# Kernel optimization log

Measured on AMD Instinct MI355X. Metric: run time of the kernel, lower is better.

Reference implementation:

```python
import jax, jax.numpy as jnp
import numpy as np

D_MODEL = 1024
NUM_HEADS = 16
D_HEAD = D_MODEL // NUM_HEADS


def setup_inputs() -> dict:
    key = jax.random.key(0)
    ks = jax.random.split(key, 9)
    s = 1.0 / np.sqrt(D_MODEL)
    inp = {"x": jax.random.normal(ks[0], (2, 2048, D_MODEL), dtype=jnp.float32)}
    for i, name in enumerate(["q", "k", "v", "o"]):
        inp[f"W_{name}"] = jax.random.uniform(ks[1 + 2 * i], (D_MODEL, D_MODEL), minval=-s, maxval=s, dtype=jnp.float32)
        inp[f"b_{name}"] = jax.random.uniform(ks[2 + 2 * i], (D_MODEL,), minval=-s, maxval=s, dtype=jnp.float32)
    return inp


def reference(x, W_q, b_q, W_k, b_k, W_v, b_v, W_o, b_o):
    B, S, _ = x.shape
    def heads(W, b):
        # [B,S,D] @ [D,D] -> [B,S,H,Dh] -> [B,H,S,Dh]
        return (x @ W.T + b).reshape(B, S, NUM_HEADS, D_HEAD).transpose(0, 2, 1, 3)
    Q, K, V = heads(W_q, b_q), heads(W_k, b_k), heads(W_v, b_v)
    scores = jnp.einsum("bhqd,bhkd->bhqk", Q, K) / jnp.sqrt(jnp.float32(D_HEAD))
    causal = jnp.tril(jnp.ones((S, S), dtype=bool))  # True = keep
    scores = jnp.where(causal, scores, -jnp.inf)
    A = jax.nn.softmax(scores, axis=-1)
    out = jnp.einsum("bhqk,bhkd->bhqd", A, V)  # [B,H,S,Dh]
    out = out.transpose(0, 2, 1, 3).reshape(B, S, D_MODEL)
    return out @ W_o.T + b_o
```

## Files before the change

kernel.cpp:

```cpp
#include <hip/hip_runtime.h>
#include <math.h>

#define D_MODEL 1024
#define NUM_HEADS 16
#define D_HEAD 64
#define SEQ 2048
#define BATCH 2
#define NROWS (BATCH * SEQ)

typedef short s8v __attribute__((ext_vector_type(8)));
typedef float f4v __attribute__((ext_vector_type(4)));

__device__ __forceinline__ short to_bf(float f) {
    union { float f; unsigned u; } x; x.f = f;
    unsigned r = x.u + 0x7fffu + ((x.u >> 16) & 1u);
    return (short)(r >> 16);
}

__device__ __forceinline__ unsigned pack_bf2(float a, float b) {
    return (unsigned)(unsigned short)to_bf(a) | ((unsigned)(unsigned short)to_bf(b) << 16);
}

__device__ __forceinline__ float fast_exp2(float x) {
    return __builtin_amdgcn_exp2f(x);
}

__device__ __forceinline__ void gld_lds16(const short* g, short* l) {
    __builtin_amdgcn_global_load_lds(
        (const __attribute__((address_space(1))) unsigned*)g,
        (__attribute__((address_space(3))) unsigned*)l, 16, 0, 0);
}

#define QSCALE 0.180336880f

__global__ __launch_bounds__(256) void cvt_fused(
    const float* __restrict__ x,  const float* __restrict__ Wq,
    const float* __restrict__ Wk, const float* __restrict__ Wv,
    const float* __restrict__ Wo,
    short* __restrict__ Xb, short* __restrict__ Wqkvb, short* __restrict__ Wob)
{
    const int NX = NROWS * D_MODEL / 4;
    const int NW = D_MODEL * D_MODEL / 4;
    int j = blockIdx.x * 256 + threadIdx.x;
    const float* src; short* dst; float sc = 1.f;
    if (j < NX)                 { src = x;  dst = Xb; }
    else if ((j -= NX) < NW)    { src = Wq; dst = Wqkvb; sc = QSCALE; }
    else if ((j -= NW) < NW)    { src = Wk; dst = Wqkvb + NW * 4; }
    else if ((j -= NW) < NW)    { src = Wv; dst = Wqkvb + NW * 8; }
    else                        { j -= NW; src = Wo; dst = Wob; }
    float4 v = ((const float4*)src)[j];
    short4 s = { to_bf(v.x * sc), to_bf(v.y * sc), to_bf(v.z * sc), to_bf(v.w * sc) };
    ((short4*)dst)[j] = s;
}

__global__ __launch_bounds__(256) void gemm_qkv(
    const short* __restrict__ Xb, const short* __restrict__ Wb,
    const float* __restrict__ B0, const float* __restrict__ B1, const float* __restrict__ B2,
    short* __restrict__ Q0, short* __restrict__ K1, short* __restrict__ V2)
{
    __shared__ __align__(16) short As[128 * 64];
    __shared__ __align__(16) short Bs[128 * 64];

    const int t    = threadIdx.x;
    const int w    = t >> 6;
    const int lane = t & 63;
    const int quad = lane >> 4;
    const int l15  = lane & 15;
    const int wm   = w & 1, wn = w >> 1;

    const int bx    = blockIdx.x;
    const int xcd   = bx & 7;
    const int g_    = bx >> 3;
    const int n_loc = g_ % 12;
    const int m_loc = g_ / 12;
    const int n0 = ((xcd >> 2) * 12 + n_loc) * 128;
    const int m0 = ((xcd & 3) * 8 + m_loc) * 128;

    const bool swapT = (n0 < 2048);

    f4v acc[4][4];
#pragma unroll
    for (int i = 0; i < 4; ++i)
#pragma unroll
        for (int j = 0; j < 4; ++j) acc[i][j] = (f4v){0.f, 0.f, 0.f, 0.f};

    for (int k0 = 0; k0 < D_MODEL; k0 += 64) {
#pragma unroll
        for (int i = 0; i < 4; ++i) {
            const int cid = i * 256 + t;
            const int row = cid >> 3, kc = cid & 7, g = kc ^ (row & 7);
            gld_lds16(&Xb[(size_t)(m0 + row) * D_MODEL + k0 + g * 8],
                      &As[(i * 256 + w * 64) * 8]);
            gld_lds16(&Wb[(size_t)(n0 + row) * D_MODEL + k0 + g * 8],
                      &Bs[(i * 256 + w * 64) * 8]);
        }
        __syncthreads();

#pragma unroll
        for (int c = 0; c < 2; ++c) {
            s8v af[4], bf[4];
            const int pos = ((c * 4 + quad) ^ (l15 & 7)) * 8;
#pragma unroll
            for (int mi = 0; mi < 4; ++mi)
                af[mi] = *(const s8v*)&As[(wm * 64 + mi * 16 + l15) * 64 + pos];
#pragma unroll
            for (int ni = 0; ni < 4; ++ni)
                bf[ni] = *(const s8v*)&Bs[(wn * 64 + ni * 16 + l15) * 64 + pos];
            if (swapT) {
#pragma unroll
                for (int mi = 0; mi < 4; ++mi)
#pragma unroll
                    for (int ni = 0; ni < 4; ++ni)
                        acc[mi][ni] = __builtin_amdgcn_mfma_f32_16x16x32_bf16(
                            bf[ni], af[mi], acc[mi][ni], 0, 0, 0);
            } else {
#pragma unroll
                for (int mi = 0; mi < 4; ++mi)
#pragma unroll
                    for (int ni = 0; ni < 4; ++ni)
                        acc[mi][ni] = __builtin_amdgcn_mfma_f32_16x16x32_bf16(
                            af[mi], bf[ni], acc[mi][ni], 0, 0, 0);
            }
        }
        __syncthreads();
    }

    if (swapT) {
        const int sel = n0 >> 10;
        const float* bias = sel == 0 ? B0 : B1;
        short* out        = sel == 0 ? Q0 : K1;
        const float bsc   = sel == 0 ? QSCALE : 1.f;
        const int nb = n0 & 1023;
#pragma unroll
        for (int ni = 0; ni < 4; ++ni) {
            const int colb = nb + wn * 64 + ni * 16 + quad * 4;
            float4 bv = *(const float4*)&bias[colb];
            const int h = colb >> 6, dh = colb & 63;
#pragma unroll
            for (int mi = 0; mi < 4; ++mi) {
                const int row = m0 + wm * 64 + mi * 16 + l15;
                const int bb = row >> 11, sl = row & (SEQ - 1);
                int2 pk;
                pk.x = (int)pack_bf2(acc[mi][ni][0] + bv.x * bsc,
                                     acc[mi][ni][1] + bv.y * bsc);
                pk.y = (int)pack_bf2(acc[mi][ni][2] + bv.z * bsc,
                                     acc[mi][ni][3] + bv.w * bsc);
                *(int2*)&out[(((size_t)(bb * NUM_HEADS + h) * SEQ) + sl) * D_HEAD + dh] = pk;
            }
        }
    } else {
        const int nb = n0 & 1023;
#pragma unroll
        for (int ni = 0; ni < 4; ++ni) {
            const int col = nb + wn * 64 + ni * 16 + l15;
            const int h = col >> 6, dh = col & 63;
            const float bv = B2[col];
#pragma unroll
            for (int mi = 0; mi < 4; ++mi) {
                const int row = m0 + wm * 64 + mi * 16 + quad * 4;
                const int bb = row >> 11, sl = row & (SEQ - 1);
                int2 pk;
                pk.x = (int)pack_bf2(acc[mi][ni][0] + bv, acc[mi][ni][1] + bv);
                pk.y = (int)pack_bf2(acc[mi][ni][2] + bv, acc[mi][ni][3] + bv);
                *(int2*)&V2[((size_t)(bb * NUM_HEADS + h) * D_HEAD + dh) * SEQ + sl] = pk;
            }
        }
    }
}

__global__ __launch_bounds__(256) void attn_mfma(
    const short* __restrict__ Qg, const short* __restrict__ Kg,
    const short* __restrict__ Vg,
    short* __restrict__ Op0, short* __restrict__ Op1, float* __restrict__ Lp)
{
    __shared__ __align__(16) short Kb[128 * 64];
    __shared__ __align__(16) short Vs[64 * 128];
    __shared__ __align__(16) short Ps[4][32 * 72];

    const int t    = threadIdx.x;
    const int w    = t >> 6;
    const int lane = t & 63;
    const int quad = lane >> 4;
    const int l15  = lane & 15;

    const int bidx = blockIdx.x;
    const int seg  = bidx >> 9;
    const int p    = bidx & 255;
    const int bh   = p >> 3;
    const int pair = p & 7;
    const int qt   = ((bidx >> 8) & 1) ? 15 - pair : pair;

    const short* qbase = Qg + (size_t)bh * SEQ * D_HEAD;
    const short* kbase = Kg + (size_t)bh * SEQ * D_HEAD;
    const short* vbase = Vg + (size_t)bh * D_HEAD * SEQ;
    const int q0 = qt * 128;
    const int qw = w * 32;

    s8v aq[2][2];
#pragma unroll
    for (int ns = 0; ns < 2; ++ns)
#pragma unroll
        for (int c = 0; c < 2; ++c)
            aq[ns][c] = *(const s8v*)&qbase[(size_t)(q0 + qw + ns * 16 + l15) * D_HEAD
                                            + c * 32 + quad * 8];

    f4v Oacc[2][4];
#pragma unroll
    for (int ms = 0; ms < 2; ++ms)
#pragma unroll
        for (int nt = 0; nt < 4; ++nt) Oacc[ms][nt] = (f4v){0.f, 0.f, 0.f, 0.f};
    float lsum[2] = {0.f, 0.f};

    for (int j = seg; j <= qt; j += 2) {
        __syncthreads();
        {
            const int k0 = j * 128;
#pragma unroll
            for (int i = 0; i < 4; ++i) {
                const int cid = i * 256 + w * 64 + lane;
                {
                    const int row = cid >> 3, pp = cid & 7, g = pp ^ (row & 7);
                    gld_lds16(&kbase[(size_t)(k0 + row) * D_HEAD + g * 8],
                              &Kb[(i * 256 + w * 64) * 8]);
                }
                {
                    const int row = cid >> 4, pp = cid & 15;
                    const int g = (pp & 8) | ((pp & 7) ^ (row & 7));
                    gld_lds16(&vbase[(size_t)row * SEQ + k0 + g * 8],
                              &Vs[(i * 256 + w * 64) * 8]);
                }
            }
        }
        __syncthreads();

        const bool diag = (j == qt);

#pragma unroll
        for (int half = 0; half < 2; ++half) {
#pragma unroll
            for (int mt = 0; mt < 4; ++mt) {
                const int krow = half * 64 + mt * 16 + l15;
                s8v ka0 = *(const s8v*)&Kb[(krow * 8 + (quad ^ (l15 & 7))) * 8];
                s8v ka1 = *(const s8v*)&Kb[(krow * 8 + ((4 + quad) ^ (l15 & 7))) * 8];
#pragma unroll
                for (int ns = 0; ns < 2; ++ns) {
                    f4v st = (f4v){0.f, 0.f, 0.f, 0.f};
                    st = __builtin_amdgcn_mfma_f32_16x16x32_bf16(ka0, aq[ns][0], st, 0, 0, 0);
                    st = __builtin_amdgcn_mfma_f32_16x16x32_bf16(ka1, aq[ns][1], st, 0, 0, 0);
                    if (diag) {
#pragma unroll
                        for (int r = 0; r < 4; ++r)
                            if (half * 64 + mt * 16 + quad * 4 + r > qw + ns * 16 + l15)
                                st[r] = -INFINITY;
                    }
                    float e0 = fast_exp2(st[0]), e1 = fast_exp2(st[1]);
                    float e2 = fast_exp2(st[2]), e3 = fast_exp2(st[3]);
                    lsum[ns] += (e0 + e1) + (e2 + e3);
                    int2 pk;
                    pk.x = (int)((__float_as_uint(e0) >> 16) | (__float_as_uint(e1) & 0xffff0000u));
                    pk.y = (int)((__float_as_uint(e2) >> 16) | (__float_as_uint(e3) & 0xffff0000u));
                    *(int2*)&Ps[w][(ns * 16 + l15) * 72 + mt * 16 + quad * 4] = pk;
                }
            }
#pragma unroll
            for (int c2 = 0; c2 < 2; ++c2) {
                s8v ap0 = *(const s8v*)&Ps[w][l15 * 72 + c2 * 32 + quad * 8];
                s8v ap1 = *(const s8v*)&Ps[w][(16 + l15) * 72 + c2 * 32 + quad * 8];
                const int g = (half * 2 + c2) * 4 + quad;
                const int pos = (g & 8) | ((g & 7) ^ (l15 & 7));
                s8v bv[4];
#pragma unroll
                for (int nt = 0; nt < 4; ++nt)
                    bv[nt] = *(const s8v*)&Vs[((nt * 16 + l15) * 16 + pos) * 8];
#pragma unroll
                for (int nt = 0; nt < 4; ++nt) {
                    Oacc[0][nt] = __builtin_amdgcn_mfma_f32_16x16x32_bf16(
                        ap0, bv[nt], Oacc[0][nt], 0, 0, 0);
                    Oacc[1][nt] = __builtin_amdgcn_mfma_f32_16x16x32_bf16(
                        ap1, bv[nt], Oacc[1][nt], 0, 0, 0);
                }
            }
        }
    }

#pragma unroll
    for (int ns = 0; ns < 2; ++ns) {
        lsum[ns] += __shfl_xor(lsum[ns], 16, 64);
        lsum[ns] += __shfl_xor(lsum[ns], 32, 64);
    }
    float* L = Lp + ((size_t)seg << 16) + (size_t)bh * SEQ;
    if (quad == 0) {
        L[q0 + qw + l15]      = lsum[0];
        L[q0 + qw + 16 + l15] = lsum[1];
    }
    short* Op = (seg ? Op1 : Op0) + (size_t)bh * SEQ * D_HEAD;
#pragma unroll
    for (int ms = 0; ms < 2; ++ms)
#pragma unroll
        for (int r = 0; r < 4; ++r) {
            const int nloc = q0 + qw + ms * 16 + quad * 4 + r;
            short* dst = Op + (size_t)nloc * D_HEAD + l15;
#pragma unroll
            for (int nt = 0; nt < 4; ++nt)
                dst[nt * 16] = to_bf(Oacc[ms][nt][r]);
        }
}

__global__ __launch_bounds__(256) void gemm_oproj(
    const short* __restrict__ Op0, const short* __restrict__ Op1,
    const float* __restrict__ Lp, const short* __restrict__ Wob,
    const float* __restrict__ bo, float* __restrict__ out)
{
    __shared__ __align__(16) short As[128 * 64];
    __shared__ __align__(16) short Bs[64 * 64];
    __shared__ float invL[NUM_HEADS * 128];

    const int t    = threadIdx.x;
    const int w    = t >> 6;
    const int lane = t & 63;
    const int quad = lane >> 4;
    const int l15  = lane & 15;
    const int wm   = w & 1, wn = w >> 1;

    const int n0 = blockIdx.x * 64;
    const int m0 = blockIdx.y * 128;
    const int bb = m0 >> 11, sloc = m0 & (SEQ - 1);

#pragma unroll
    for (int ii = 0; ii < 8; ++ii) {
        const int idx = t * 8 + ii;
        const int hh = idx >> 7, sl = idx & 127;
        const size_t loff = (size_t)(bb * NUM_HEADS + hh) * SEQ + sloc + sl;
        invL[idx] = 1.f / (Lp[loff] + Lp[65536 + loff]);
    }
    __syncthreads();

    f4v acc[4][2];
#pragma unroll
    for (int i = 0; i < 4; ++i)
#pragma unroll
        for (int j = 0; j < 2; ++j) acc[i][j] = (f4v){0.f, 0.f, 0.f, 0.f};

    for (int k0 = 0; k0 < D_MODEL; k0 += 64) {
        const int h = k0 >> 6;
#pragma unroll
        for (int i = 0; i < 2; ++i) {
            const int cid = i * 256 + w * 64 + lane;
            const int row = cid >> 3, pp = cid & 7, g = pp ^ (row & 7);
            gld_lds16(&Wob[(size_t)(n0 + row) * D_MODEL + k0 + g * 8],
                      &Bs[(i * 256 + w * 64) * 8]);
        }
        const size_t obase = ((size_t)(bb * NUM_HEADS + h) * SEQ + sloc) * D_HEAD;
#pragma unroll
        for (int i = 0; i < 4; ++i) {
            const int cid = i * 256 + t;
            const int row = cid >> 3, pp = cid & 7, g = pp ^ (row & 7);
            const size_t off = obase + (size_t)row * D_HEAD + g * 8;
            int4 a0 = *(const int4*)&Op0[off];
            int4 a1 = *(const int4*)&Op1[off];
            const float inv = invL[h * 128 + row];
            const unsigned* u0 = (const unsigned*)&a0;
            const unsigned* u1 = (const unsigned*)&a1;
            int4 o;
#pragma unroll
            for (int d = 0; d < 4; ++d) {
                float lo = (__uint_as_float(u0[d] << 16) +
                            __uint_as_float(u1[d] << 16)) * inv;
                float hi = (__uint_as_float(u0[d] & 0xffff0000u) +
                            __uint_as_float(u1[d] & 0xffff0000u)) * inv;
                ((unsigned*)&o)[d] = (__float_as_uint(lo) >> 16) |
                                     (__float_as_uint(hi) & 0xffff0000u);
            }
            *(int4*)&As[cid * 8] = o;
        }
        __syncthreads();

#pragma unroll
        for (int c = 0; c < 2; ++c) {
            s8v af[4], bf[2];
            const int pos = ((c * 4 + quad) ^ (l15 & 7)) * 8;
#pragma unroll
            for (int mi = 0; mi < 4; ++mi)
                af[mi] = *(const s8v*)&As[(wm * 64 + mi * 16 + l15) * 64 + pos];
#pragma unroll
            for (int ni = 0; ni < 2; ++ni)
                bf[ni] = *(const s8v*)&Bs[(wn * 32 + ni * 16 + l15) * 64 + pos];
#pragma unroll
            for (int mi = 0; mi < 4; ++mi)
#pragma unroll
                for (int ni = 0; ni < 2; ++ni)
                    acc[mi][ni] = __builtin_amdgcn_mfma_f32_16x16x32_bf16(
                        af[mi], bf[ni], acc[mi][ni], 0, 0, 0);
        }
        __syncthreads();
    }

#pragma unroll
    for (int ni = 0; ni < 2; ++ni) {
        const int col = n0 + wn * 32 + ni * 16 + l15;
        const float bv = bo[col];
#pragma unroll
        for (int mi = 0; mi < 4; ++mi)
#pragma unroll
            for (int r = 0; r < 4; ++r) {
                const int row = m0 + wm * 64 + mi * 16 + quad * 4 + r;
                out[(size_t)row * D_MODEL + col] = acc[mi][ni][r] + bv;
            }
    }
}

extern "C" void kernel_launch(void* const* d_in, const int* in_sizes, int n_in,
                              void* d_out, int out_size, void* d_ws, size_t ws_size,
                              hipStream_t stream)
{
    const float* x  = (const float*)d_in[0];
    const float* Wq = (const float*)d_in[1];
    const float* bq = (const float*)d_in[2];
    const float* Wk = (const float*)d_in[3];
    const float* bk = (const float*)d_in[4];
    const float* Wv = (const float*)d_in[5];
    const float* bv = (const float*)d_in[6];
    const float* Wo = (const float*)d_in[7];
    const float* bo = (const float*)d_in[8];
    float* out = (float*)d_out;

    short* wsp = (short*)d_ws;
    const size_t MAT = (size_t)NROWS * D_MODEL;
    short* Qb    = wsp;
    short* Kbg   = Qb + MAT;
    short* Vtb   = Kbg + MAT;
    short* Xb    = Vtb + 2 * MAT;
    short* Wqkvb = Xb + MAT;
    short* Wob   = Wqkvb + 3 * D_MODEL * D_MODEL;
    short* Op0   = Xb;
    short* Op1   = Wob + D_MODEL * D_MODEL;
    float* Lp    = (float*)(Op1 + MAT);

    cvt_fused<<<8192, 256, 0, stream>>>(x, Wq, Wk, Wv, Wo, Xb, Wqkvb, Wob);

    gemm_qkv<<<768, 256, 0, stream>>>(Xb, Wqkvb, bq, bk, bv, Qb, Kbg, Vtb);

    attn_mfma<<<1024, 256, 0, stream>>>(Qb, Kbg, Vtb, Op0, Op1, Lp);

    gemm_oproj<<<dim3(D_MODEL / 64, NROWS / 128), 256, 0, stream>>>(
        Op0, Op1, Lp, Wob, bo, out);
}
```

Before: 197.7 us.

## Load K and V fragments directly from global memory instead of staging in LDS

Removes the shared-memory staging of K and V tiles and the two block-wide barriers per key block in the attention kernel. Each wave now reads its K and V MFMA operand fragments directly from global memory, relying on L1/L2 caching. This drops LDS traffic and synchronisation, but each of the four waves now fetches the same K/V data separately, which multiplies global/cache traffic and exposes load latency with no explicit prefetch.

```diff
diff --git a/kernel.cpp b/kernel.cpp
--- a/kernel.cpp
+++ b/kernel.cpp
@@ -173,8 +173,6 @@
     const short* __restrict__ Vg,
     short* __restrict__ Op0, short* __restrict__ Op1, float* __restrict__ Lp)
 {
-    __shared__ __align__(16) short Kb[128 * 64];
-    __shared__ __align__(16) short Vs[64 * 128];
     __shared__ __align__(16) short Ps[4][32 * 72];
 
     const int t    = threadIdx.x;
@@ -212,41 +210,26 @@
     float lsum[2] = {0.f, 0.f};
 
     for (int j = seg; j <= qt; j += 2) {
-        __syncthreads();
-        {
-            const int k0 = j * 128;
-#pragma unroll
-            for (int i = 0; i < 4; ++i) {
-                const int cid = i * 256 + w * 64 + lane;
-                {
-                    const int row = cid >> 3, pp = cid & 7, g = pp ^ (row & 7);
-                    gld_lds16(&kbase[(size_t)(k0 + row) * D_HEAD + g * 8],
-                              &Kb[(i * 256 + w * 64) * 8]);
-                }
-                {
-                    const int row = cid >> 4, pp = cid & 15;
-                    const int g = (pp & 8) | ((pp & 7) ^ (row & 7));
-                    gld_lds16(&vbase[(size_t)row * SEQ + k0 + g * 8],
-                              &Vs[(i * 256 + w * 64) * 8]);
-                }
-            }
-        }
-        __syncthreads();
-
+        const int k0 = j * 128;
         const bool diag = (j == qt);
 
 #pragma unroll
         for (int half = 0; half < 2; ++half) {
+            s8v ka[4][2];
 #pragma unroll
             for (int mt = 0; mt < 4; ++mt) {
-                const int krow = half * 64 + mt * 16 + l15;
-                s8v ka0 = *(const s8v*)&Kb[(krow * 8 + (quad ^ (l15 & 7))) * 8];
-                s8v ka1 = *(const s8v*)&Kb[(krow * 8 + ((4 + quad) ^ (l15 & 7))) * 8];
+                const int krow = k0 + half * 64 + mt * 16 + l15;
+                const short* kr = &kbase[(size_t)krow * D_HEAD + quad * 8];
+                ka[mt][0] = *(const s8v*)kr;
+                ka[mt][1] = *(const s8v*)(kr + 32);
+            }
+#pragma unroll
+            for (int mt = 0; mt < 4; ++mt) {
 #pragma unroll
                 for (int ns = 0; ns < 2; ++ns) {
                     f4v st = (f4v){0.f, 0.f, 0.f, 0.f};
-                    st = __builtin_amdgcn_mfma_f32_16x16x32_bf16(ka0, aq[ns][0], st, 0, 0, 0);
-                    st = __builtin_amdgcn_mfma_f32_16x16x32_bf16(ka1, aq[ns][1], st, 0, 0, 0);
+                    st = __builtin_amdgcn_mfma_f32_16x16x32_bf16(ka[mt][0], aq[ns][0], st, 0, 0, 0);
+                    st = __builtin_amdgcn_mfma_f32_16x16x32_bf16(ka[mt][1], aq[ns][1], st, 0, 0, 0);
                     if (diag) {
 #pragma unroll
                         for (int r = 0; r < 4; ++r)
@@ -266,12 +249,11 @@
             for (int c2 = 0; c2 < 2; ++c2) {
                 s8v ap0 = *(const s8v*)&Ps[w][l15 * 72 + c2 * 32 + quad * 8];
                 s8v ap1 = *(const s8v*)&Ps[w][(16 + l15) * 72 + c2 * 32 + quad * 8];
-                const int g = (half * 2 + c2) * 4 + quad;
-                const int pos = (g & 8) | ((g & 7) ^ (l15 & 7));
                 s8v bv[4];
 #pragma unroll
                 for (int nt = 0; nt < 4; ++nt)
-                    bv[nt] = *(const s8v*)&Vs[((nt * 16 + l15) * 16 + pos) * 8];
+                    bv[nt] = *(const s8v*)&vbase[(size_t)(nt * 16 + l15) * SEQ
+                                                 + k0 + half * 64 + c2 * 32 + quad * 8];
 #pragma unroll
                 for (int nt = 0; nt < 4; ++nt) {
                     Oacc[0][nt] = __builtin_amdgcn_mfma_f32_16x16x32_bf16(
```

New measurement: 225.8 us. 1.14x slower.
